# Optimization experiments

Measured on AMD Instinct MI355X. Metric: run time of the kernel, lower is better.

Reference implementation:

```python
import jax, jax.numpy as jnp
import numpy as np

NEAR, FAR = 2.0, 6.0
N_SAMPLES = 64
L_PTS, L_DIR = 10, 4
INF_DELTA = 1e10


def posenc(x, L):
    # x: [..., 3] -> [..., 3 + 6*L] (identity + sin/cos at 2^l frequencies)
    freqs = 2.0 ** jnp.arange(L, dtype=x.dtype)              # [L]
    ang = x[..., None, :] * freqs[:, None]                   # [..., L, 3]
    enc = jnp.concatenate([jnp.sin(ang), jnp.cos(ang)], axis=-1)  # [..., L, 6]
    return jnp.concatenate([x, enc.reshape(x.shape[:-1] + (L * 6,))], axis=-1)


def setup_inputs() -> dict:
    key = jax.random.key(0)
    ks = jax.random.split(key, 12)
    R, D, DH = 4096, 256, 128
    PE_P, PE_D = 3 + 6 * L_PTS, 3 + 6 * L_DIR  # 63, 27

    def w(k, shape):
        fan_in = shape[0]
        return jax.random.normal(k, shape, dtype=jnp.float32) / np.sqrt(fan_in)

    return {
        "xyz": jax.random.normal(ks[0], (1, R, 3), dtype=jnp.float32),
        "viewdirs": jax.random.normal(ks[1], (1, R, 3), dtype=jnp.float32),
        "W1": w(ks[2], (PE_P, D)), "b1": jnp.zeros((D,), jnp.float32),
        "W2": w(ks[3], (D, D)),    "b2": jnp.zeros((D,), jnp.float32),
        "W3": w(ks[4], (D, D)),    "b3": jnp.zeros((D,), jnp.float32),
        "Wsig": w(ks[5], (D, 1)),  "bsig": jnp.zeros((1,), jnp.float32),
        "Wfeat": w(ks[6], (D, D)), "bfeat": jnp.zeros((D,), jnp.float32),
        "Wdir": w(ks[7], (D + PE_D, DH)), "bdir": jnp.zeros((DH,), jnp.float32),
        "Wrgb": w(ks[8], (DH, 3)), "brgb": jnp.zeros((3,), jnp.float32),
    }


def reference(xyz, viewdirs, W1, b1, W2, b2, W3, b3, Wsig, bsig,
              Wfeat, bfeat, Wdir, bdir, Wrgb, brgb):
    xyz = xyz[0]          # [R, 3] (batch dim squeezed as in render_coarse)
    vd = viewdirs[0]
    vd = vd / jnp.linalg.norm(vd, axis=-1, keepdims=True)
    R = xyz.shape[0]

    # Evenly spaced samples between near and far (perturb=0 -> deterministic)
    t = jnp.linspace(0.0, 1.0, N_SAMPLES, dtype=xyz.dtype)
    samples = NEAR * (1.0 - t) + FAR * t                     # [N]
    samples = jnp.broadcast_to(samples, (R, N_SAMPLES))      # [R, N]
    delta = jnp.concatenate(
        [samples[:, 1:] - samples[:, :-1],
         jnp.full((R, 1), INF_DELTA, dtype=samples.dtype)], axis=-1)  # [R, N]

    # Sample points along each ray
    pts = xyz[:, None, :] + samples[..., None] * vd[:, None, :]  # [R, N, 3]

    # NeRF MLP: positional-encoded points -> density + view-dep color
    pe = posenc(pts, L_PTS)                                   # [R, N, 63]
    de = posenc(vd, L_DIR)                                    # [R, 27]
    h = jax.nn.relu(pe @ W1 + b1)
    h = jax.nn.relu(h @ W2 + b2)
    h = jax.nn.relu(h @ W3 + b3)                              # [R, N, 256]
    density = (h @ Wsig + bsig)[..., 0]                       # [R, N]
    feat = h @ Wfeat + bfeat                                  # [R, N, 256]
    de_b = jnp.broadcast_to(de[:, None, :], (R, N_SAMPLES, de.shape[-1]))
    hd = jax.nn.relu(jnp.concatenate([feat, de_b], axis=-1) @ Wdir + bdir)
    rgb = jax.nn.sigmoid(hd @ Wrgb + brgb)                    # [R, N, 3]

    # Volume rendering (alpha compositing with cumprod transmittance)
    sigma = jax.nn.relu(density)
    alpha = 1.0 - jnp.exp(-sigma * delta)                     # [R, N]
    T = jnp.concatenate(
        [jnp.ones((R, 1), alpha.dtype),
         jnp.cumprod(1.0 - alpha[:, :-1], axis=-1)], axis=-1)
    w = T * alpha                                             # [R, N]
    rgb_map = jnp.sum(w[..., None] * rgb, axis=-2)            # [R, 3]
    alpha_map = jnp.sum(w, axis=-1, keepdims=True)            # [R, 1]
    rgb_map = rgb_map + (1.0 - alpha_map)                     # white_bkgd
    depth_map = jnp.sum(w * samples, axis=-1)                 # [R]
    return rgb_map, depth_map, alpha_map
```

## Files before the change

### kernel.cpp

```cpp
#include <hip/hip_runtime.h>
#include <hip/hip_bf16.h>
#include <math.h>


typedef unsigned short u16;
typedef unsigned int   u32;
typedef __bf16 bf16x8 __attribute__((ext_vector_type(8)));
typedef float  f32x4  __attribute__((ext_vector_type(4)));

#define HI_STRIDE 296
#define LO_STRIDE 264
#define NROW 64

__device__ __align__(16) u16 g_whi[249856];
__device__ __align__(16) u16 g_wlo[147456];

constexpr int OFF_W1 = 0;
constexpr int OFF_W2 = 16384;
constexpr int OFF_W3 = 81920;
constexpr int OFF_WF = 147456;
constexpr int OFF_WD = 212992;

static __device__ __forceinline__ float bf2f(u16 u) {
  return __uint_as_float(((u32)u) << 16);
}
static __device__ __forceinline__ u16 f2bf(float f) {
  u32 x = __float_as_uint(f);
  return (u16)((x + 0x7FFFu + ((x >> 16) & 1u)) >> 16);
}
static __device__ __forceinline__ float wash(float x) {
  return (x == x) ? x : 0.0f;
}

struct alignas(8) U16x4 { u16 x, y, z, w; };

__global__ void repack_kernel(const float* __restrict__ w1, const float* __restrict__ w2,
                              const float* __restrict__ w3, const float* __restrict__ wf,
                              const float* __restrict__ wd) {
  int e = blockIdx.x * 256 + threadIdx.x;
  const float* src; int K, N, ks, base;
  if (e < 81920)       { if (e < 16384) { src = w1; K = 63;  N = 256; ks = 2; base = OFF_W1; }
                         else           { src = w2; K = 256; N = 256; ks = 8; base = OFF_W2; } }
  else if (e < 147456) { src = w3; K = 256; N = 256; ks = 8; base = OFF_W3; }
  else if (e < 212992) { src = wf; K = 256; N = 256; ks = 8; base = OFF_WF; }
  else                 { src = wd; K = 283; N = 128; ks = 9; base = OFF_WD; }
  int le   = e - base;
  int f    = le >> 9, pos = le & 511;
  int lane = pos >> 3, j = pos & 7;
  int t    = f / ks,  s = f - t * ks;
  int k    = s * 32 + ((lane >> 4) << 3) + j;
  int n    = (t << 4) + (lane & 15);
  float v  = (k < K) ? src[k * N + n] : 0.0f;
  u16 h    = f2bf(v);
  g_whi[e] = h;
  if (e < 147456) g_wlo[e] = f2bf(v - bf2f(h));
}

template<int KS, int NT, int RT, bool RELU, bool SPLIT>
static __device__ __forceinline__ void mlp_layer(u16* hi, u16* lo,
                                                 const u16* __restrict__ wh_,
                                                 const u16* __restrict__ wl_,
                                                 const float* __restrict__ bias,
                                                 int rg, int cg, int lane) {
  f32x4 acc[RT][NT];
#pragma unroll
  for (int rt = 0; rt < RT; ++rt)
#pragma unroll
    for (int nt = 0; nt < NT; ++nt) {
      f32x4 z = {0.0f, 0.0f, 0.0f, 0.0f};
      acc[rt][nt] = z;
    }
  const int l15 = lane & 15, q = lane >> 4;
#pragma unroll
  for (int s = 0; s < KS; ++s) {
    bf16x8 ah[RT], al[RT];
#pragma unroll
    for (int rt = 0; rt < RT; ++rt) {
      const int row = (rg * RT + rt) * 16 + l15;
      ah[rt] = *reinterpret_cast<const bf16x8*>(&hi[row * HI_STRIDE + s * 32 + q * 8]);
      if (SPLIT)
        al[rt] = *reinterpret_cast<const bf16x8*>(&lo[row * LO_STRIDE + s * 32 + q * 8]);
    }
    bf16x8 wh[NT], wl[NT];
#pragma unroll
    for (int nt = 0; nt < NT; ++nt) {
      const int t = cg * NT + nt;
      wh[nt] = *reinterpret_cast<const bf16x8*>(&wh_[(t * KS + s) * 512 + lane * 8]);
      if (SPLIT)
        wl[nt] = *reinterpret_cast<const bf16x8*>(&wl_[(t * KS + s) * 512 + lane * 8]);
    }
#pragma unroll
    for (int rt = 0; rt < RT; ++rt)
#pragma unroll
      for (int nt = 0; nt < NT; ++nt) {
        acc[rt][nt] = __builtin_amdgcn_mfma_f32_16x16x32_bf16(
            wh[nt], ah[rt], acc[rt][nt], 0, 0, 0);
        if (SPLIT) {
          acc[rt][nt] = __builtin_amdgcn_mfma_f32_16x16x32_bf16(
              wh[nt], al[rt], acc[rt][nt], 0, 0, 0);
          acc[rt][nt] = __builtin_amdgcn_mfma_f32_16x16x32_bf16(
              wl[nt], ah[rt], acc[rt][nt], 0, 0, 0);
        }
      }
  }
  __syncthreads();
#pragma unroll
  for (int nt = 0; nt < NT; ++nt) {
    const int nb = (cg * NT + nt) * 16 + q * 4;
    const float b0 = bias[nb + 0], b1 = bias[nb + 1];
    const float b2 = bias[nb + 2], b3 = bias[nb + 3];
#pragma unroll
    for (int rt = 0; rt < RT; ++rt) {
      const int row = (rg * RT + rt) * 16 + l15;
      float v0 = acc[rt][nt][0] + b0;
      float v1 = acc[rt][nt][1] + b1;
      float v2 = acc[rt][nt][2] + b2;
      float v3 = acc[rt][nt][3] + b3;
      if (RELU) {
        v0 = fmaxf(v0, 0.0f); v1 = fmaxf(v1, 0.0f);
        v2 = fmaxf(v2, 0.0f); v3 = fmaxf(v3, 0.0f);
      }
      U16x4 oh; oh.x = f2bf(v0); oh.y = f2bf(v1); oh.z = f2bf(v2); oh.w = f2bf(v3);
      *reinterpret_cast<U16x4*>(&hi[row * HI_STRIDE + nb]) = oh;
      if (SPLIT) {
        U16x4 ol;
        ol.x = f2bf(v0 - bf2f(oh.x)); ol.y = f2bf(v1 - bf2f(oh.y));
        ol.z = f2bf(v2 - bf2f(oh.z)); ol.w = f2bf(v3 - bf2f(oh.w));
        *reinterpret_cast<U16x4*>(&lo[row * LO_STRIDE + nb]) = ol;
      }
    }
  }
  __syncthreads();
}

__global__ __launch_bounds__(512, 4)
void nerf_kernel(const float* __restrict__ xyz, const float* __restrict__ vdirs,
                 const float* __restrict__ b1, const float* __restrict__ b2,
                 const float* __restrict__ b3, const float* __restrict__ wsig,
                 const float* __restrict__ bsig, const float* __restrict__ bfeat,
                 const float* __restrict__ bdir, const float* __restrict__ wrgb,
                 const float* __restrict__ brgb, float* __restrict__ out) {
  __shared__ u16  s_hi[NROW * HI_STRIDE];
  __shared__ u16  s_lo[NROW * LO_STRIDE];
  __shared__ float s_geo[6];
  __shared__ float s_de[32];

  const int tid  = threadIdx.x;
  const int wave = tid >> 6;
  const int lane = tid & 63;
  const int rg   = wave >> 2;
  const int cg   = wave & 3;

  if (tid == 0) {
    int rgI = blockIdx.x;
    float vx = vdirs[rgI * 3 + 0];
    float vy = vdirs[rgI * 3 + 1];
    float vz = vdirs[rgI * 3 + 2];
    float inv = 1.0f / sqrtf(vx * vx + vy * vy + vz * vz + 1e-20f);
    s_geo[0] = xyz[rgI * 3 + 0];
    s_geo[1] = xyz[rgI * 3 + 1];
    s_geo[2] = xyz[rgI * 3 + 2];
    s_geo[3] = vx * inv;
    s_geo[4] = vy * inv;
    s_geo[5] = vz * inv;
  }
  __syncthreads();

  if (tid < 32) {
    float val = 0.0f;
    if (tid < 3) val = s_geo[3 + tid];
    else if (tid < 27) {
      int fi = tid - 3, l = fi / 6, m = fi % 6;
      int ii = (m < 3) ? m : m - 3;
      float ang = s_geo[3 + ii] * (float)(1 << l);
      val = (m < 3) ? sinf(ang) : cosf(ang);
    }
    s_de[tid] = val;
  }

  {
    int row = tid >> 3, c8 = tid & 7;
    float t  = (float)row * (1.0f / 63.0f);
    float ts = 2.0f * (1.0f - t) + 6.0f * t;
    float p[3];
    p[0] = s_geo[0] + ts * s_geo[3];
    p[1] = s_geo[1] + ts * s_geo[4];
    p[2] = s_geo[2] + ts * s_geo[5];
#pragma unroll
    for (int j = 0; j < 8; ++j) {
      int f = c8 * 8 + j;
      float val;
      if (f < 3) val = p[f];
      else if (f == 63) val = 0.0f;
      else {
        int fi = f - 3, l = fi / 6, m = fi % 6;
        int ii = (m < 3) ? m : m - 3;
        float ang = p[ii] * (float)(1 << l);
        val = (m < 3) ? sinf(ang) : cosf(ang);
      }
      u16 h = f2bf(val);
      s_hi[row * HI_STRIDE + f] = h;
      s_lo[row * LO_STRIDE + f] = f2bf(val - bf2f(h));
    }
  }
  __syncthreads();

  mlp_layer<2, 4, 2, true, true>(s_hi, s_lo, g_whi + OFF_W1, g_wlo + OFF_W1,
                                 b1, rg, cg, lane);
  mlp_layer<8, 4, 2, true, true>(s_hi, s_lo, g_whi + OFF_W2, g_wlo + OFF_W2,
                                 b2, rg, cg, lane);
  mlp_layer<8, 4, 2, true, true>(s_hi, s_lo, g_whi + OFF_W3, g_wlo + OFF_W3,
                                 b3, rg, cg, lane);

  float my_den = 0.0f;
  if (tid < 64) {
    float a = 0.0f;
    const float4* wp = reinterpret_cast<const float4*>(wsig);
#pragma unroll 8
    for (int k4 = 0; k4 < 64; ++k4) {
      U16x4 h = *reinterpret_cast<const U16x4*>(&s_hi[tid * HI_STRIDE + k4 * 4]);
      U16x4 l = *reinterpret_cast<const U16x4*>(&s_lo[tid * LO_STRIDE + k4 * 4]);
      float4 w = wp[k4];
      a += (bf2f(h.x) + bf2f(l.x)) * w.x + (bf2f(h.y) + bf2f(l.y)) * w.y
         + (bf2f(h.z) + bf2f(l.z)) * w.z + (bf2f(h.w) + bf2f(l.w)) * w.w;
    }
    my_den = wash(a + bsig[0]);
  }

  mlp_layer<8, 4, 2, false, false>(s_hi, s_lo, g_whi + OFF_WF, g_wlo,
                                   bfeat, rg, cg, lane);

  {
    int row = tid >> 3, i0 = (tid & 7) * 4;
#pragma unroll
    for (int j = 0; j < 4; ++j)
      s_hi[row * HI_STRIDE + 256 + i0 + j] = f2bf(s_de[i0 + j]);
  }
  __syncthreads();

  mlp_layer<9, 2, 2, true, false>(s_hi, s_lo, g_whi + OFF_WD, g_wlo,
                                  bdir, rg, cg, lane);

  float r0 = 0.0f, r1 = 0.0f, r2 = 0.0f;
  if (tid < 64) {
    float a0 = brgb[0], a1 = brgb[1], a2 = brgb[2];
#pragma unroll 8
    for (int k = 0; k < 128; ++k) {
      float hv = bf2f(s_hi[tid * HI_STRIDE + k]);
      a0 += hv * wrgb[k * 3 + 0];
      a1 += hv * wrgb[k * 3 + 1];
      a2 += hv * wrgb[k * 3 + 2];
    }
    a0 = wash(a0); a1 = wash(a1); a2 = wash(a2);
    r0 = 1.0f / (1.0f + expf(-a0));
    r1 = 1.0f / (1.0f + expf(-a1));
    r2 = 1.0f / (1.0f + expf(-a2));
  }

  if (wave == 0) {
    int rgI = blockIdx.x;
    float t  = (float)lane * (1.0f / 63.0f);
    float ts = 2.0f * (1.0f - t) + 6.0f * t;
    float delta;
    if (lane < 63) {
      float t2 = (float)(lane + 1) * (1.0f / 63.0f);
      delta = (2.0f * (1.0f - t2) + 6.0f * t2) - ts;
    } else delta = 1e10f;
    float sig = fmaxf(my_den, 0.0f);
    float sd  = fminf(sig * delta, 60.0f);
    float incl = sd;
#pragma unroll
    for (int o = 1; o < 64; o <<= 1) {
      float v = __shfl_up(incl, o, 64);
      if (lane >= o) incl += v;
    }
    float excl  = fminf(fmaxf(incl - sd, 0.0f), 60.0f);
    float T     = expf(-excl);
    float alpha = 1.0f - expf(-sd);
    float w     = T * alpha;
    float sw = w, swr = w * r0, swg = w * r1, swb = w * r2, swd = w * ts;
#pragma unroll
    for (int o = 32; o > 0; o >>= 1) {
      sw  += __shfl_xor(sw,  o, 64);
      swr += __shfl_xor(swr, o, 64);
      swg += __shfl_xor(swg, o, 64);
      swb += __shfl_xor(swb, o, 64);
      swd += __shfl_xor(swd, o, 64);
    }
    if (lane == 0) {
      float bg = 1.0f - sw;
      out[rgI * 3 + 0]  = swr + bg;
      out[rgI * 3 + 1]  = swg + bg;
      out[rgI * 3 + 2]  = swb + bg;
      out[12288 + rgI]  = swd;
      out[16384 + rgI]  = sw;
    }
  }
}

extern "C" void kernel_launch(void* const* d_in, const int* in_sizes, int n_in,
                              void* d_out, int out_size, void* d_ws, size_t ws_size,
                              hipStream_t stream) {
  const float* xyz   = (const float*)d_in[0];
  const float* vdirs = (const float*)d_in[1];
  const float* W1    = (const float*)d_in[2];
  const float* b1    = (const float*)d_in[3];
  const float* W2    = (const float*)d_in[4];
  const float* b2    = (const float*)d_in[5];
  const float* W3    = (const float*)d_in[6];
  const float* b3    = (const float*)d_in[7];
  const float* Wsig  = (const float*)d_in[8];
  const float* bsig  = (const float*)d_in[9];
  const float* Wfeat = (const float*)d_in[10];
  const float* bfeat = (const float*)d_in[11];
  const float* Wdir  = (const float*)d_in[12];
  const float* bdir  = (const float*)d_in[13];
  const float* Wrgb  = (const float*)d_in[14];
  const float* brgb  = (const float*)d_in[15];
  float* out = (float*)d_out;

  repack_kernel<<<dim3(976), dim3(256), 0, stream>>>(W1, W2, W3, Wfeat, Wdir);
  nerf_kernel<<<dim3(4096), dim3(512), 0, stream>>>(
      xyz, vdirs, b1, b2, b3, Wsig, bsig, bfeat, bdir, Wrgb, brgb, out);
}
```

Baseline: 394.1 us.

## Use packed hardware bf16 conversion and regroup MFMA issue order in MLP layers

Replaces the software round-to-nearest bf16 conversion with the packed v_cvt_pk_bf16_f32 instruction in layer epilogues, positional encoding and direction-feature writes, and stores the packed pairs as 32-bit words. Inside mlp_layer the k-loop is no longer unrolled, and the hi*hi, hi*lo and lo*hi MFMA groups are issued as separate passes so consecutive MFMAs do not depend on the same accumulator. The aim is to cut VALU work in epilogues and to cut register pressure and MFMA dependency stalls. The cost is less compiler freedom to prefetch the next k-step's loads across iterations.

```diff
diff --git a/kernel.cpp b/kernel.cpp
--- a/kernel.cpp
+++ b/kernel.cpp
@@ -27,6 +27,11 @@
 static __device__ __forceinline__ u16 f2bf(float f) {
   u32 x = __float_as_uint(f);
   return (u16)((x + 0x7FFFu + ((x >> 16) & 1u)) >> 16);
+}
+static __device__ __forceinline__ u32 cvt_pk_bf16(float a, float b) {
+  u32 r;
+  asm("v_cvt_pk_bf16_f32 %0, %1, %2" : "=v"(r) : "v"(a), "v"(b));
+  return r;
 }
 static __device__ __forceinline__ float wash(float x) {
   return (x == x) ? x : 0.0f;
@@ -71,7 +76,7 @@
       acc[rt][nt] = z;
     }
   const int l15 = lane & 15, q = lane >> 4;
-#pragma unroll
+#pragma unroll 1
   for (int s = 0; s < KS; ++s) {
     bf16x8 ah[RT], al[RT];
 #pragma unroll
@@ -90,18 +95,25 @@
         wl[nt] = *reinterpret_cast<const bf16x8*>(&wl_[(t * KS + s) * 512 + lane * 8]);
     }
 #pragma unroll
-    for (int rt = 0; rt < RT; ++rt)
-#pragma unroll
-      for (int nt = 0; nt < NT; ++nt) {
+    for (int nt = 0; nt < NT; ++nt)
+#pragma unroll
+      for (int rt = 0; rt < RT; ++rt)
         acc[rt][nt] = __builtin_amdgcn_mfma_f32_16x16x32_bf16(
             wh[nt], ah[rt], acc[rt][nt], 0, 0, 0);
-        if (SPLIT) {
+    if (SPLIT) {
+#pragma unroll
+      for (int nt = 0; nt < NT; ++nt)
+#pragma unroll
+        for (int rt = 0; rt < RT; ++rt)
           acc[rt][nt] = __builtin_amdgcn_mfma_f32_16x16x32_bf16(
               wh[nt], al[rt], acc[rt][nt], 0, 0, 0);
+#pragma unroll
+      for (int nt = 0; nt < NT; ++nt)
+#pragma unroll
+        for (int rt = 0; rt < RT; ++rt)
           acc[rt][nt] = __builtin_amdgcn_mfma_f32_16x16x32_bf16(
               wl[nt], ah[rt], acc[rt][nt], 0, 0, 0);
-        }
-      }
+    }
   }
   __syncthreads();
 #pragma unroll
@@ -120,13 +132,17 @@
         v0 = fmaxf(v0, 0.0f); v1 = fmaxf(v1, 0.0f);
         v2 = fmaxf(v2, 0.0f); v3 = fmaxf(v3, 0.0f);
       }
-      U16x4 oh; oh.x = f2bf(v0); oh.y = f2bf(v1); oh.z = f2bf(v2); oh.w = f2bf(v3);
-      *reinterpret_cast<U16x4*>(&hi[row * HI_STRIDE + nb]) = oh;
+      u32 h01 = cvt_pk_bf16(v0, v1);
+      u32 h23 = cvt_pk_bf16(v2, v3);
+      *reinterpret_cast<uint2*>(&hi[row * HI_STRIDE + nb]) = make_uint2(h01, h23);
       if (SPLIT) {
-        U16x4 ol;
-        ol.x = f2bf(v0 - bf2f(oh.x)); ol.y = f2bf(v1 - bf2f(oh.y));
-        ol.z = f2bf(v2 - bf2f(oh.z)); ol.w = f2bf(v3 - bf2f(oh.w));
-        *reinterpret_cast<U16x4*>(&lo[row * LO_STRIDE + nb]) = ol;
+        float l0 = v0 - __uint_as_float(h01 << 16);
+        float l1 = v1 - __uint_as_float(h01 & 0xFFFF0000u);
+        float l2 = v2 - __uint_as_float(h23 << 16);
+        float l3 = v3 - __uint_as_float(h23 & 0xFFFF0000u);
+        u32 lo01 = cvt_pk_bf16(l0, l1);
+        u32 lo23 = cvt_pk_bf16(l2, l3);
+        *reinterpret_cast<uint2*>(&lo[row * LO_STRIDE + nb]) = make_uint2(lo01, lo23);
       }
     }
   }
@@ -186,21 +202,28 @@
     p[0] = s_geo[0] + ts * s_geo[3];
     p[1] = s_geo[1] + ts * s_geo[4];
     p[2] = s_geo[2] + ts * s_geo[5];
+    float val[8];
 #pragma unroll
     for (int j = 0; j < 8; ++j) {
       int f = c8 * 8 + j;
-      float val;
-      if (f < 3) val = p[f];
-      else if (f == 63) val = 0.0f;
+      if (f < 3) val[j] = p[f];
+      else if (f == 63) val[j] = 0.0f;
       else {
         int fi = f - 3, l = fi / 6, m = fi % 6;
         int ii = (m < 3) ? m : m - 3;
         float ang = p[ii] * (float)(1 << l);
-        val = (m < 3) ? sinf(ang) : cosf(ang);
+        val[j] = (m < 3) ? sinf(ang) : cosf(ang);
       }
-      u16 h = f2bf(val);
-      s_hi[row * HI_STRIDE + f] = h;
-      s_lo[row * LO_STRIDE + f] = f2bf(val - bf2f(h));
+    }
+    u32* hp = reinterpret_cast<u32*>(&s_hi[row * HI_STRIDE + c8 * 8]);
+    u32* lp = reinterpret_cast<u32*>(&s_lo[row * LO_STRIDE + c8 * 8]);
+#pragma unroll
+    for (int jp = 0; jp < 4; ++jp) {
+      u32 h = cvt_pk_bf16(val[2 * jp], val[2 * jp + 1]);
+      float l0 = val[2 * jp]     - __uint_as_float(h << 16);
+      float l1 = val[2 * jp + 1] - __uint_as_float(h & 0xFFFF0000u);
+      hp[jp] = h;
+      lp[jp] = cvt_pk_bf16(l0, l1);
     }
   }
   __syncthreads();
@@ -232,9 +255,10 @@
 
   {
     int row = tid >> 3, i0 = (tid & 7) * 4;
-#pragma unroll
-    for (int j = 0; j < 4; ++j)
-      s_hi[row * HI_STRIDE + 256 + i0 + j] = f2bf(s_de[i0 + j]);
+    u32 d01 = cvt_pk_bf16(s_de[i0 + 0], s_de[i0 + 1]);
+    u32 d23 = cvt_pk_bf16(s_de[i0 + 2], s_de[i0 + 3]);
+    u32* dp = reinterpret_cast<u32*>(&s_hi[row * HI_STRIDE + 256 + i0]);
+    dp[0] = d01; dp[1] = d23;
   }
   __syncthreads();
 
```

New measurement: 386.2 us. 2.0% less time.
